# Kernel tuning notes

Measured on AMD Instinct MI355X. Metric: run time of the kernel, lower is better.

## Reference

```python
import jax, jax.numpy as jnp
import numpy as np

N_NODES = 50000
IN_CH = 512
OUT_CH = 512
N_EDGES = 800000


def setup_inputs() -> dict:
    key = jax.random.key(0)
    ks = jax.random.split(key, 6)
    x = jax.random.normal(ks[0], (N_NODES, IN_CH), dtype=jnp.float32)
    edge_index = jax.random.randint(ks[1], (2, N_EDGES), 0, N_NODES, dtype=jnp.int64)
    edge_index_2 = jax.random.randint(ks[2], (2, N_EDGES), 0, N_NODES, dtype=jnp.int64)
    W1 = jax.random.normal(ks[3], (IN_CH, OUT_CH), dtype=jnp.float32) * (1.0 / np.sqrt(IN_CH))
    b1 = jnp.zeros((OUT_CH,), dtype=jnp.float32)
    W2 = jax.random.normal(ks[4], (IN_CH, OUT_CH), dtype=jnp.float32) * (1.0 / np.sqrt(IN_CH))
    b2 = jnp.zeros((OUT_CH,), dtype=jnp.float32)
    return {"x": x, "edge_index": edge_index, "edge_index_2": edge_index_2,
            "W1": W1, "b1": b1, "W2": W2, "b2": b2}


def _sgconv(x, edge_index, W, b, K=2):
    # PyG SGConv: K rounds of D^-1/2 (A+I) D^-1/2 propagation, then Linear.
    N = x.shape[0]
    loops = jnp.arange(N, dtype=edge_index.dtype)
    row = jnp.concatenate([edge_index[0], loops])  # source nodes
    col = jnp.concatenate([edge_index[1], loops])  # destination nodes
    deg = jax.ops.segment_sum(jnp.ones_like(col, dtype=x.dtype), col, num_segments=N)
    deg_inv_sqrt = jnp.where(deg > 0, jnp.where(deg > 0, deg, 1.0) ** -0.5, 0.0)
    norm = deg_inv_sqrt[row] * deg_inv_sqrt[col]  # [E+N]
    h = x
    for _ in range(K):
        h = jax.ops.segment_sum(h[row] * norm[:, None], col, num_segments=N)
    return h @ W + b


def reference(x, edge_index, edge_index_2, W1, b1, W2, b2):
    x1 = _sgconv(x, edge_index, W1, b1)
    x2 = _sgconv(x, edge_index_2, W2, b2)
    logits = jax.nn.softmax(x1, axis=1)
    logits_2 = jax.nn.softmax(x2, axis=1)
    predictions = jnp.argmax(logits, axis=1)
    return (logits, logits_2, predictions)
```

## Files before the change

### kernel.cpp

```cpp
#include <hip/hip_runtime.h>
#include <hip/hip_bf16.h>
#include <cstdint>
#include <cstddef>

#define N_NODES 50000
#define N_EDGES 800000
#define CH 512

typedef __attribute__((ext_vector_type(8))) short bf16x8;
typedef __attribute__((ext_vector_type(4))) float f32x4;

__device__ inline unsigned short f2b(float f) {
    __hip_bfloat16 h = __float2bfloat16(f);
    return *(unsigned short*)&h;
}
__device__ inline float blo(unsigned int u) {
    union { unsigned int i; float f; } v; v.i = u << 16; return v.f;
}
__device__ inline float bhi(unsigned int u) {
    union { unsigned int i; float f; } v; v.i = u & 0xffff0000u; return v.f;
}
__device__ inline unsigned int pack2(unsigned short a, unsigned short b) {
    return (unsigned)a | ((unsigned)b << 16);
}


__global__ __launch_bounds__(256) void count_col(const int* __restrict__ col, int* __restrict__ cnt) {
    int e = blockIdx.x * 256 + threadIdx.x;
    if (e < N_EDGES) atomicAdd(&cnt[col[e]], 1);
}

__global__ __launch_bounds__(1024) void scan_offsets(const int* __restrict__ cnt, int* __restrict__ offs,
                                                     float* __restrict__ dinv) {
    __shared__ int wsum[16];
    __shared__ int s_carry;
    int tid = threadIdx.x;
    int lane = tid & 63, wid = tid >> 6;
    if (tid == 0) s_carry = 0;
    __syncthreads();
    const int n = N_NODES;
    for (int c0 = 0; c0 < n; c0 += 1024) {
        int i = c0 + tid;
        int v = (i < n) ? cnt[i] : 0;
        if (i < n) dinv[i] = rsqrtf((float)(v + 1));
        int incl = v;
        #pragma unroll
        for (int d = 1; d < 64; d <<= 1) {
            int t = __shfl_up(incl, d, 64);
            if (lane >= d) incl += t;
        }
        if (lane == 63) wsum[wid] = incl;
        __syncthreads();
        int wbase = 0;
        for (int w = 0; w < wid; ++w) wbase += wsum[w];
        int excl = s_carry + wbase + incl - v;
        if (i < n) offs[i] = excl;
        int ctot = wbase + incl;
        __syncthreads();
        if (tid == 1023) s_carry += ctot;
        __syncthreads();
    }
    if (tid == 0) offs[n] = s_carry;
}

__global__ __launch_bounds__(256) void fill_csr(const int* __restrict__ edges,
                                                const int* __restrict__ offs,
                                                int* __restrict__ cursor,
                                                const float* __restrict__ dinv,
                                                int* __restrict__ srcs,
                                                float* __restrict__ enorm) {
    int e = blockIdx.x * 256 + threadIdx.x;
    if (e >= N_EDGES) return;
    int r = edges[e];
    int c = edges[N_EDGES + e];
    int p = offs[c] + atomicAdd(&cursor[c], 1);
    srcs[p] = r;
    enorm[p] = dinv[r] * dinv[c];
}


__global__ __launch_bounds__(256) void convert_x_bf16(const float* __restrict__ x, unsigned short* __restrict__ xb) {
    int i8 = blockIdx.x * 256 + threadIdx.x;
    const float4* x4 = (const float4*)x;
    float4 a = x4[2 * i8], b = x4[2 * i8 + 1];
    unsigned int o[4];
    o[0] = pack2(f2b(a.x), f2b(a.y));
    o[1] = pack2(f2b(a.z), f2b(a.w));
    o[2] = pack2(f2b(b.x), f2b(b.y));
    o[3] = pack2(f2b(b.z), f2b(b.w));
    ((uint4*)xb)[i8] = make_uint4(o[0], o[1], o[2], o[3]);
}

__global__ __launch_bounds__(256) void convert_w_t(const float* __restrict__ W, unsigned short* __restrict__ Wt) {
    int id = blockIdx.x * 256 + threadIdx.x;
    int k = id >> 9, n = id & 511;
    Wt[(size_t)n * 512 + k] = f2b(W[(size_t)k * 512 + n]);
}

__global__ __launch_bounds__(256) void convert_w_t_split(const float* __restrict__ W,
                                                         unsigned short* __restrict__ Wth,
                                                         unsigned short* __restrict__ Wtl) {
    int id = blockIdx.x * 256 + threadIdx.x;
    int k = id >> 9, n = id & 511;
    float f = W[(size_t)k * 512 + n];
    unsigned short hb = f2b(f);
    union { unsigned int u; float ff; } t; t.u = (unsigned)hb << 16;
    float lo = f - t.ff;
    Wth[(size_t)n * 512 + k] = hb;
    Wtl[(size_t)n * 512 + k] = f2b(lo);
}


__global__ __launch_bounds__(128) void propagate(const float* __restrict__ h, float* __restrict__ out,
                                                 const int* __restrict__ offs,
                                                 const int* __restrict__ srcs,
                                                 const float* __restrict__ enorm,
                                                 const float* __restrict__ dinv) {
    int node = blockIdx.x;
    int t = threadIdx.x;
    const float4* h4 = (const float4*)h;
    float di = dinv[node];
    float w0 = di * di;
    float4 v = h4[(size_t)node * 128 + t];
    float4 acc = make_float4(v.x * w0, v.y * w0, v.z * w0, v.w * w0);
    int e0 = offs[node], e1 = offs[node + 1];
    int e = e0;
    int eu = e0 + ((e1 - e0) & ~7);
    for (; e < eu; e += 8) {
        int s[8]; float w[8];
        #pragma unroll
        for (int q = 0; q < 8; ++q) { s[q] = srcs[e + q]; w[q] = enorm[e + q]; }
        float4 u[8];
        #pragma unroll
        for (int q = 0; q < 8; ++q) u[q] = h4[(size_t)s[q] * 128 + t];
        #pragma unroll
        for (int q = 0; q < 8; ++q) {
            acc.x += u[q].x * w[q]; acc.y += u[q].y * w[q];
            acc.z += u[q].z * w[q]; acc.w += u[q].w * w[q];
        }
    }
    for (; e < e1; ++e) {
        int s = srcs[e];
        float w = enorm[e];
        float4 u = h4[(size_t)s * 128 + t];
        acc.x += u.x * w; acc.y += u.y * w; acc.z += u.z * w; acc.w += u.w * w;
    }
    ((float4*)out)[(size_t)node * 128 + t] = acc;
}


__global__ __launch_bounds__(128) void propagate_bf16(const unsigned short* __restrict__ hb,
                                                      unsigned short* __restrict__ outb,
                                                      const int* __restrict__ offs,
                                                      const int* __restrict__ srcs,
                                                      const float* __restrict__ enorm,
                                                      const float* __restrict__ dinv) {
    int node = blockIdx.x * 2 + (threadIdx.x >> 6);
    int lane = threadIdx.x & 63;
    const uint4* h16 = (const uint4*)hb;
    float di = dinv[node];
    float w0 = di * di;
    float acc[8];
    uint4 sv = h16[(size_t)node * 64 + lane];
    acc[0] = blo(sv.x) * w0; acc[1] = bhi(sv.x) * w0;
    acc[2] = blo(sv.y) * w0; acc[3] = bhi(sv.y) * w0;
    acc[4] = blo(sv.z) * w0; acc[5] = bhi(sv.z) * w0;
    acc[6] = blo(sv.w) * w0; acc[7] = bhi(sv.w) * w0;
    int e0 = offs[node], e1 = offs[node + 1];
    int e = e0;
    int eu = e0 + ((e1 - e0) & ~7);
    for (; e < eu; e += 8) {
        int s[8]; float w[8];
        #pragma unroll
        for (int q = 0; q < 8; ++q) { s[q] = srcs[e + q]; w[q] = enorm[e + q]; }
        uint4 u[8];
        #pragma unroll
        for (int q = 0; q < 8; ++q) u[q] = h16[(size_t)s[q] * 64 + lane];
        #pragma unroll
        for (int q = 0; q < 8; ++q) {
            acc[0] += blo(u[q].x) * w[q]; acc[1] += bhi(u[q].x) * w[q];
            acc[2] += blo(u[q].y) * w[q]; acc[3] += bhi(u[q].y) * w[q];
            acc[4] += blo(u[q].z) * w[q]; acc[5] += bhi(u[q].z) * w[q];
            acc[6] += blo(u[q].w) * w[q]; acc[7] += bhi(u[q].w) * w[q];
        }
    }
    for (; e < e1; ++e) {
        int s = srcs[e];
        float w = enorm[e];
        uint4 u = h16[(size_t)s * 64 + lane];
        acc[0] += blo(u.x) * w; acc[1] += bhi(u.x) * w;
        acc[2] += blo(u.y) * w; acc[3] += bhi(u.y) * w;
        acc[4] += blo(u.z) * w; acc[5] += bhi(u.z) * w;
        acc[6] += blo(u.w) * w; acc[7] += bhi(u.w) * w;
    }
    unsigned int o0 = pack2(f2b(acc[0]), f2b(acc[1]));
    unsigned int o1 = pack2(f2b(acc[2]), f2b(acc[3]));
    unsigned int o2 = pack2(f2b(acc[4]), f2b(acc[5]));
    unsigned int o3 = pack2(f2b(acc[6]), f2b(acc[7]));
    ((uint4*)outb)[(size_t)node * 64 + lane] = make_uint4(o0, o1, o2, o3);
}


#define BM2 128
#define BN2 256
#define BK2 32
#define LDP 40

__global__ __launch_bounds__(512) void gemm_bf16(const unsigned short* __restrict__ Ab,
                                                 const unsigned short* __restrict__ Wt,
                                                 const float* __restrict__ bias,
                                                 float* __restrict__ C) {
    __shared__ short Alds[BM2 * LDP];
    __shared__ short Blds[BN2 * LDP];
    int tid = threadIdx.x;
    int lane = tid & 63;
    int wid = tid >> 6;
    int wm = wid & 1;
    int wn = wid >> 1;
    int bm = blockIdx.x * BM2;
    int bn = blockIdx.y * BN2;

    f32x4 acc[4][4] = {};

    int arow = tid >> 2, ak8 = (tid & 3) * 8;
    int brow = tid >> 1, bk16 = (tid & 1) * 16;
    int ga = bm + arow;
    bool aval = ga < N_NODES;

    for (int k0 = 0; k0 < CH; k0 += BK2) {
        {
            uint4 v = make_uint4(0u, 0u, 0u, 0u);
            if (aval) v = *(const uint4*)&Ab[(size_t)ga * CH + k0 + ak8];
            *(uint4*)&Alds[arow * LDP + ak8] = v;
        }
        {
            const unsigned short* s = &Wt[(size_t)(bn + brow) * CH + k0 + bk16];
            *(uint4*)&Blds[brow * LDP + bk16] = *(const uint4*)s;
            *(uint4*)&Blds[brow * LDP + bk16 + 8] = *(const uint4*)(s + 8);
        }
        __syncthreads();

        bf16x8 af[4], bf[4];
        #pragma unroll
        for (int mt = 0; mt < 4; ++mt)
            af[mt] = *(const bf16x8*)&Alds[(wm * 64 + mt * 16 + (lane & 15)) * LDP + (lane >> 4) * 8];
        #pragma unroll
        for (int nt = 0; nt < 4; ++nt)
            bf[nt] = *(const bf16x8*)&Blds[(wn * 64 + nt * 16 + (lane & 15)) * LDP + (lane >> 4) * 8];
        #pragma unroll
        for (int mt = 0; mt < 4; ++mt)
            #pragma unroll
            for (int nt = 0; nt < 4; ++nt)
                acc[mt][nt] = __builtin_amdgcn_mfma_f32_16x16x32_bf16(af[mt], bf[nt], acc[mt][nt], 0, 0, 0);
        __syncthreads();
    }

    #pragma unroll
    for (int mt = 0; mt < 4; ++mt) {
        #pragma unroll
        for (int nt = 0; nt < 4; ++nt) {
            int col = bn + wn * 64 + nt * 16 + (lane & 15);
            float bv = bias[col];
            #pragma unroll
            for (int r = 0; r < 4; ++r) {
                int row = bm + wm * 64 + mt * 16 + (lane >> 4) * 4 + r;
                if (row < N_NODES) C[(size_t)row * CH + col] = acc[mt][nt][r] + bv;
            }
        }
    }
}


#define BM3 128
#define BN3 256
#define BK3 32
#define LDP3 40

__global__ __launch_bounds__(512) void gemm_bf16x3(const float* __restrict__ A,
                                                   const unsigned short* __restrict__ Wth,
                                                   const unsigned short* __restrict__ Wtl,
                                                   const float* __restrict__ bias,
                                                   float* __restrict__ C) {
    __shared__ short Ah[BM3 * LDP3];
    __shared__ short Al[BM3 * LDP3];
    __shared__ short Bh[BN3 * LDP3];
    __shared__ short Bl[BN3 * LDP3];
    int tid = threadIdx.x;
    int lane = tid & 63;
    int wid = tid >> 6;
    int wm = wid & 1;
    int wn = wid >> 1;
    int bm = blockIdx.x * BM3;
    int bn = blockIdx.y * BN3;

    f32x4 acc[4][4] = {};

    int arow = tid >> 2, ak8 = (tid & 3) * 8;
    int brow = tid >> 1, bk16 = (tid & 1) * 16;
    int ga = bm + arow;
    bool aval = ga < N_NODES;

    for (int k0 = 0; k0 < CH; k0 += BK3) {
        {
            const float* src = &A[(size_t)ga * CH + k0 + ak8];
            float4 f0 = aval ? *(const float4*)(src)     : make_float4(0.f, 0.f, 0.f, 0.f);
            float4 f1 = aval ? *(const float4*)(src + 4) : make_float4(0.f, 0.f, 0.f, 0.f);
            float fs[8] = {f0.x, f0.y, f0.z, f0.w, f1.x, f1.y, f1.z, f1.w};
            unsigned short h[8], l[8];
            #pragma unroll
            for (int j = 0; j < 8; ++j) {
                unsigned short hb = f2b(fs[j]);
                union { unsigned int u; float ff; } t; t.u = (unsigned)hb << 16;
                float lo = fs[j] - t.ff;
                h[j] = hb;
                l[j] = f2b(lo);
            }
            *(uint4*)&Ah[arow * LDP3 + ak8] =
                make_uint4(pack2(h[0], h[1]), pack2(h[2], h[3]), pack2(h[4], h[5]), pack2(h[6], h[7]));
            *(uint4*)&Al[arow * LDP3 + ak8] =
                make_uint4(pack2(l[0], l[1]), pack2(l[2], l[3]), pack2(l[4], l[5]), pack2(l[6], l[7]));
        }
        {
            const unsigned short* sh = &Wth[(size_t)(bn + brow) * CH + k0 + bk16];
            const unsigned short* sl = &Wtl[(size_t)(bn + brow) * CH + k0 + bk16];
            *(uint4*)&Bh[brow * LDP3 + bk16]     = *(const uint4*)sh;
            *(uint4*)&Bh[brow * LDP3 + bk16 + 8] = *(const uint4*)(sh + 8);
            *(uint4*)&Bl[brow * LDP3 + bk16]     = *(const uint4*)sl;
            *(uint4*)&Bl[brow * LDP3 + bk16 + 8] = *(const uint4*)(sl + 8);
        }
        __syncthreads();

        bf16x8 afh[4], afl[4], bfh[4], bfl[4];
        #pragma unroll
        for (int mt = 0; mt < 4; ++mt) {
            int off = (wm * 64 + mt * 16 + (lane & 15)) * LDP3 + (lane >> 4) * 8;
            afh[mt] = *(const bf16x8*)&Ah[off];
            afl[mt] = *(const bf16x8*)&Al[off];
        }
        #pragma unroll
        for (int nt = 0; nt < 4; ++nt) {
            int off = (wn * 64 + nt * 16 + (lane & 15)) * LDP3 + (lane >> 4) * 8;
            bfh[nt] = *(const bf16x8*)&Bh[off];
            bfl[nt] = *(const bf16x8*)&Bl[off];
        }
        #pragma unroll
        for (int mt = 0; mt < 4; ++mt)
            #pragma unroll
            for (int nt = 0; nt < 4; ++nt) {
                acc[mt][nt] = __builtin_amdgcn_mfma_f32_16x16x32_bf16(afh[mt], bfh[nt], acc[mt][nt], 0, 0, 0);
                acc[mt][nt] = __builtin_amdgcn_mfma_f32_16x16x32_bf16(afl[mt], bfh[nt], acc[mt][nt], 0, 0, 0);
                acc[mt][nt] = __builtin_amdgcn_mfma_f32_16x16x32_bf16(afh[mt], bfl[nt], acc[mt][nt], 0, 0, 0);
            }
        __syncthreads();
    }

    #pragma unroll
    for (int mt = 0; mt < 4; ++mt) {
        #pragma unroll
        for (int nt = 0; nt < 4; ++nt) {
            int col = bn + wn * 64 + nt * 16 + (lane & 15);
            float bv = bias[col];
            #pragma unroll
            for (int r = 0; r < 4; ++r) {
                int row = bm + wm * 64 + mt * 16 + (lane >> 4) * 4 + r;
                if (row < N_NODES) C[(size_t)row * CH + col] = acc[mt][nt][r] + bv;
            }
        }
    }
}


#define GAP_THR 2.0e-4f
#define SUSP_CAP 49999

__global__ __launch_bounds__(256) void softmax_rows(const float* __restrict__ X, float* __restrict__ P,
                                                    float* __restrict__ preds,
                                                    int* __restrict__ susp_cnt,
                                                    int* __restrict__ susp_rows) {
    int row = blockIdx.x * 4 + (threadIdx.x >> 6);
    int lane = threadIdx.x & 63;
    if (row >= N_NODES) return;
    const float4* x4 = (const float4*)(X + (size_t)row * CH);
    float4 v0 = x4[lane];
    float4 v1 = x4[lane + 64];
    float vals[8] = {v0.x, v0.y, v0.z, v0.w, v1.x, v1.y, v1.z, v1.w};
    float m = vals[0];
    float m2 = -INFINITY;
    int mi = lane * 4;
    #pragma unroll
    for (int j = 1; j < 8; ++j) {
        int c = (j < 4) ? (lane * 4 + j) : (256 + lane * 4 + (j - 4));
        if (vals[j] > m) { m2 = m; m = vals[j]; mi = c; }
        else if (vals[j] > m2) { m2 = vals[j]; }
    }
    #pragma unroll
    for (int d = 32; d > 0; d >>= 1) {
        float om = __shfl_xor(m, d, 64);
        int oi = __shfl_xor(mi, d, 64);
        float om2 = __shfl_xor(m2, d, 64);
        if (om > m || (om == m && oi < mi)) {
            m2 = fmaxf(m, om2);
            m = om; mi = oi;
        } else {
            m2 = fmaxf(m2, om);
        }
    }
    float s = 0.f;
    float ex[8];
    #pragma unroll
    for (int j = 0; j < 8; ++j) { ex[j] = __expf(vals[j] - m); s += ex[j]; }
    #pragma unroll
    for (int d = 32; d > 0; d >>= 1) s += __shfl_xor(s, d, 64);
    float inv = 1.0f / s;
    float4 o0 = make_float4(ex[0] * inv, ex[1] * inv, ex[2] * inv, ex[3] * inv);
    float4 o1 = make_float4(ex[4] * inv, ex[5] * inv, ex[6] * inv, ex[7] * inv);
    float4* p4 = (float4*)(P + (size_t)row * CH);
    p4[lane] = o0;
    p4[lane + 64] = o1;
    if (preds != nullptr && lane == 0) {
        preds[row] = (float)mi;
        if (m - m2 < GAP_THR) {
            int p = atomicAdd(susp_cnt, 1);
            if (p < SUSP_CAP) susp_rows[p] = row;
        }
    }
}


__global__ __launch_bounds__(256) void fix_preds(const float* __restrict__ A, const float* __restrict__ W,
                                                 const float* __restrict__ bias,
                                                 const int* __restrict__ susp_cnt,
                                                 const int* __restrict__ susp_rows,
                                                 float* __restrict__ preds) {
    __shared__ float rowbuf[8][512];
    __shared__ float rbest[8][4];
    __shared__ int ridx[8][4];
    int cnt = *susp_cnt;
    if (cnt > SUSP_CAP) cnt = SUSP_CAP;
    int tid = threadIdx.x, lane = tid & 63, wid = tid >> 6;
    for (int base = blockIdx.x * 8; base < cnt; base += gridDim.x * 8) {
        int nr = min(8, cnt - base);
        __syncthreads();
        for (int r = 0; r < nr; ++r) {
            int row = susp_rows[base + r];
            if (tid < 128) ((float4*)rowbuf[r])[tid] = ((const float4*)&A[(size_t)row * 512])[tid];
        }
        __syncthreads();
        float best[8]; int bidx[8];
        #pragma unroll
        for (int r = 0; r < 8; ++r) { best[r] = -INFINITY; bidx[r] = 0; }
        for (int cc = 0; cc < 2; ++cc) {
            int c = cc * 256 + tid;
            float bv = bias[c];
            float s[8];
            #pragma unroll
            for (int r = 0; r < 8; ++r) s[r] = bv;
            #pragma unroll 8
            for (int k = 0; k < 512; ++k) {
                float w = W[(size_t)k * 512 + c];
                #pragma unroll
                for (int r = 0; r < 8; ++r) s[r] += rowbuf[r][k] * w;
            }
            #pragma unroll
            for (int r = 0; r < 8; ++r)
                if (s[r] > best[r]) { best[r] = s[r]; bidx[r] = c; }
        }
        #pragma unroll
        for (int r = 0; r < 8; ++r) {
            float b = best[r]; int i = bidx[r];
            #pragma unroll
            for (int d = 32; d > 0; d >>= 1) {
                float ob = __shfl_xor(b, d, 64);
                int oi = __shfl_xor(i, d, 64);
                if (ob > b || (ob == b && oi < i)) { b = ob; i = oi; }
            }
            if (lane == 0) { rbest[r][wid] = b; ridx[r][wid] = i; }
        }
        __syncthreads();
        if (tid < nr) {
            int r = tid;
            float b = rbest[r][0]; int i = ridx[r][0];
            #pragma unroll
            for (int w = 1; w < 4; ++w) {
                if (rbest[r][w] > b || (rbest[r][w] == b && ridx[r][w] < i)) { b = rbest[r][w]; i = ridx[r][w]; }
            }
            preds[susp_rows[base + r]] = (float)i;
        }
    }
}


extern "C" void kernel_launch(void* const* d_in, const int* in_sizes, int n_in,
                              void* d_out, int out_size, void* d_ws, size_t ws_size,
                              hipStream_t stream) {
    const float* x  = (const float*)d_in[0];
    const int*   e1 = (const int*)d_in[1];
    const int*   e2 = (const int*)d_in[2];
    const float* W1 = (const float*)d_in[3];
    const float* b1 = (const float*)d_in[4];
    const float* W2 = (const float*)d_in[5];
    const float* b2 = (const float*)d_in[6];

    float* out     = (float*)d_out;
    float* logits1 = out;
    float* logits2 = out + (size_t)N_NODES * CH;
    float* preds   = out + 2 * (size_t)N_NODES * CH;

    const size_t NEED = 109600016;
    if (ws_size < NEED) return;

    char* ws = (char*)d_ws;
    float* A      = (float*)(ws);
    int*   cnt    = (int*)(ws + 102400000);
    int*   offs   = (int*)(ws + 102600000);
    int*   cursor = (int*)(ws + 102800016);
    float* dinv   = (float*)(ws + 103000016);
    int*   srcs   = (int*)(ws + 103200016);
    float* enorm  = (float*)(ws + 106400016);

    unsigned short* xb  = (unsigned short*)logits1;
    unsigned short* Wtb = (unsigned short*)((char*)logits1 + 51200000);
    unsigned short* h1b = (unsigned short*)A;
    unsigned short* h2b = (unsigned short*)((char*)A + 51200000);

    unsigned short* Wt1h = (unsigned short*)srcs;
    unsigned short* Wt1l = (unsigned short*)enorm;
    int* susp_cnt  = (int*)cursor;
    int* susp_rows = (int*)cursor + 1;

    {
        hipMemsetAsync(cnt, 0, N_NODES * sizeof(int), stream);
        hipMemsetAsync(cursor, 0, N_NODES * sizeof(int), stream);
        count_col<<<(N_EDGES + 255) / 256, 256, 0, stream>>>(e2 + N_EDGES, cnt);
        scan_offsets<<<1, 1024, 0, stream>>>(cnt, offs, dinv);
        fill_csr<<<(N_EDGES + 255) / 256, 256, 0, stream>>>(e2, offs, cursor, dinv, srcs, enorm);

        convert_x_bf16<<<(N_NODES * CH / 8 + 255) / 256, 256, 0, stream>>>(x, xb);
        convert_w_t<<<(512 * 512) / 256, 256, 0, stream>>>(W2, Wtb);

        propagate_bf16<<<N_NODES / 2, 128, 0, stream>>>(xb, h1b, offs, srcs, enorm, dinv);
        propagate_bf16<<<N_NODES / 2, 128, 0, stream>>>(h1b, h2b, offs, srcs, enorm, dinv);

        dim3 g((N_NODES + BM2 - 1) / BM2, CH / BN2);
        gemm_bf16<<<g, 512, 0, stream>>>(h2b, Wtb, b2, logits2);
        softmax_rows<<<N_NODES / 4, 256, 0, stream>>>(logits2, logits2, nullptr, nullptr, nullptr);
    }

    {
        hipMemsetAsync(cnt, 0, N_NODES * sizeof(int), stream);
        hipMemsetAsync(cursor, 0, N_NODES * sizeof(int), stream);
        count_col<<<(N_EDGES + 255) / 256, 256, 0, stream>>>(e1 + N_EDGES, cnt);
        scan_offsets<<<1, 1024, 0, stream>>>(cnt, offs, dinv);
        fill_csr<<<(N_EDGES + 255) / 256, 256, 0, stream>>>(e1, offs, cursor, dinv, srcs, enorm);

        propagate<<<N_NODES, 128, 0, stream>>>(x, logits1, offs, srcs, enorm, dinv);
        propagate<<<N_NODES, 128, 0, stream>>>(logits1, A, offs, srcs, enorm, dinv);

        convert_w_t_split<<<(512 * 512) / 256, 256, 0, stream>>>(W1, Wt1h, Wt1l);
        hipMemsetAsync(susp_cnt, 0, sizeof(int), stream);

        dim3 g((N_NODES + BM3 - 1) / BM3, CH / BN3);
        gemm_bf16x3<<<g, 512, 0, stream>>>(A, Wt1h, Wt1l, b1, logits1);
        softmax_rows<<<N_NODES / 4, 256, 0, stream>>>(logits1, logits1, preds, susp_cnt, susp_rows);
        fix_preds<<<400, 256, 0, stream>>>(A, W1, b1, susp_cnt, susp_rows, preds);
    }
}
```

Measured before the change: 1.676 ms.

## Build both graphs' CSR together with a multi-block parallel scan

Replaces the single-block, 1024-thread serial-chunk prefix scan with a three-stage multi-block scan. The stages are a per-block scan, a scan of the block sums, and an add-back fused with the dinv computation and the cursor reset. The count and fill kernels for both edge sets are merged into single launches, with graph 2's CSR arrays placed in the not-yet-written logits2 output buffer. This removes a serialized single-CU scan and several launches and memsets. It relies on logits2 staying untouched until graph 2's propagation has finished.

```diff
diff --git a/kernel.cpp b/kernel.cpp
--- a/kernel.cpp
+++ b/kernel.cpp
@@ -6,6 +6,7 @@
 #define N_NODES 50000
 #define N_EDGES 800000
 #define CH 512
+#define SCAN_NB 49
 
 typedef __attribute__((ext_vector_type(8))) short bf16x8;
 typedef __attribute__((ext_vector_type(4))) float f32x4;
@@ -25,57 +26,108 @@
 }
 
 
-__global__ __launch_bounds__(256) void count_col(const int* __restrict__ col, int* __restrict__ cnt) {
-    int e = blockIdx.x * 256 + threadIdx.x;
-    if (e < N_EDGES) atomicAdd(&cnt[col[e]], 1);
-}
-
-__global__ __launch_bounds__(1024) void scan_offsets(const int* __restrict__ cnt, int* __restrict__ offs,
-                                                     float* __restrict__ dinv) {
-    __shared__ int wsum[16];
-    __shared__ int s_carry;
-    int tid = threadIdx.x;
+__global__ __launch_bounds__(256) void count_both(const int* __restrict__ e1, const int* __restrict__ e2,
+                                                  int* __restrict__ cnt1, int* __restrict__ cnt2) {
+    int t = blockIdx.x * 256 + threadIdx.x;
+    if (t < N_EDGES) {
+        atomicAdd(&cnt1[e1[N_EDGES + t]], 1);
+    } else if (t < 2 * N_EDGES) {
+        int e = t - N_EDGES;
+        atomicAdd(&cnt2[e2[N_EDGES + e]], 1);
+    }
+}
+
+__global__ __launch_bounds__(256) void scan_s1(const int* __restrict__ c1, const int* __restrict__ c2,
+                                               int* __restrict__ o1, int* __restrict__ o2,
+                                               int* __restrict__ bsum) {
+    const int* cnt = blockIdx.y ? c2 : c1;
+    int* offs = blockIdx.y ? o2 : o1;
+    int* bs = bsum + blockIdx.y * 64;
+    int b = blockIdx.x, tid = threadIdx.x;
     int lane = tid & 63, wid = tid >> 6;
-    if (tid == 0) s_carry = 0;
+    int i0 = b * 1024 + tid * 4;
+    int v[4];
+    #pragma unroll
+    for (int j = 0; j < 4; ++j) { int i = i0 + j; v[j] = (i < N_NODES) ? cnt[i] : 0; }
+    int tsum = v[0] + v[1] + v[2] + v[3];
+    int incl = tsum;
+    #pragma unroll
+    for (int d = 1; d < 64; d <<= 1) {
+        int t = __shfl_up(incl, d, 64);
+        if (lane >= d) incl += t;
+    }
+    __shared__ int wsum[4];
+    if (lane == 63) wsum[wid] = incl;
     __syncthreads();
-    const int n = N_NODES;
-    for (int c0 = 0; c0 < n; c0 += 1024) {
-        int i = c0 + tid;
-        int v = (i < n) ? cnt[i] : 0;
-        if (i < n) dinv[i] = rsqrtf((float)(v + 1));
-        int incl = v;
-        #pragma unroll
-        for (int d = 1; d < 64; d <<= 1) {
-            int t = __shfl_up(incl, d, 64);
-            if (lane >= d) incl += t;
-        }
-        if (lane == 63) wsum[wid] = incl;
-        __syncthreads();
-        int wbase = 0;
-        for (int w = 0; w < wid; ++w) wbase += wsum[w];
-        int excl = s_carry + wbase + incl - v;
-        if (i < n) offs[i] = excl;
-        int ctot = wbase + incl;
-        __syncthreads();
-        if (tid == 1023) s_carry += ctot;
-        __syncthreads();
-    }
-    if (tid == 0) offs[n] = s_carry;
-}
-
-__global__ __launch_bounds__(256) void fill_csr(const int* __restrict__ edges,
-                                                const int* __restrict__ offs,
-                                                int* __restrict__ cursor,
-                                                const float* __restrict__ dinv,
-                                                int* __restrict__ srcs,
-                                                float* __restrict__ enorm) {
-    int e = blockIdx.x * 256 + threadIdx.x;
-    if (e >= N_EDGES) return;
-    int r = edges[e];
-    int c = edges[N_EDGES + e];
-    int p = offs[c] + atomicAdd(&cursor[c], 1);
-    srcs[p] = r;
-    enorm[p] = dinv[r] * dinv[c];
+    int wbase = 0;
+    for (int w = 0; w < wid; ++w) wbase += wsum[w];
+    int run = wbase + incl - tsum;
+    #pragma unroll
+    for (int j = 0; j < 4; ++j) { int i = i0 + j; if (i < N_NODES) offs[i] = run; run += v[j]; }
+    if (tid == 255) bs[b] = wbase + incl;
+}
+
+__global__ __launch_bounds__(64) void scan_s2(int* __restrict__ bsum,
+                                              int* __restrict__ o1, int* __restrict__ o2) {
+    int* bs = bsum + blockIdx.y * 64;
+    int* offs = blockIdx.y ? o2 : o1;
+    int t = threadIdx.x;
+    int v = (t < SCAN_NB) ? bs[t] : 0;
+    int incl = v;
+    #pragma unroll
+    for (int d = 1; d < 64; d <<= 1) {
+        int u = __shfl_up(incl, d, 64);
+        if (t >= d) incl += u;
+    }
+    if (t < SCAN_NB) bs[t] = incl - v;
+    if (t == 63) offs[N_NODES] = incl;
+}
+
+__global__ __launch_bounds__(256) void scan_s3(const int* __restrict__ c1, const int* __restrict__ c2,
+                                               int* __restrict__ o1, int* __restrict__ o2,
+                                               float* __restrict__ d1, float* __restrict__ d2,
+                                               int* __restrict__ cur1, int* __restrict__ cur2,
+                                               const int* __restrict__ bsum) {
+    const int* cnt = blockIdx.y ? c2 : c1;
+    int* offs = blockIdx.y ? o2 : o1;
+    float* dinv = blockIdx.y ? d2 : d1;
+    int* cursor = blockIdx.y ? cur2 : cur1;
+    int add = bsum[blockIdx.y * 64 + blockIdx.x];
+    int i0 = blockIdx.x * 1024 + threadIdx.x * 4;
+    #pragma unroll
+    for (int j = 0; j < 4; ++j) {
+        int i = i0 + j;
+        if (i < N_NODES) {
+            offs[i] += add;
+            dinv[i] = rsqrtf((float)(cnt[i] + 1));
+            cursor[i] = 0;
+        }
+    }
+}
+
+__global__ __launch_bounds__(256) void fill_both(const int* __restrict__ e1,
+                                                 const int* __restrict__ offs1, int* __restrict__ cur1,
+                                                 const float* __restrict__ dinv1,
+                                                 int* __restrict__ srcs1, float* __restrict__ enorm1,
+                                                 const int* __restrict__ e2,
+                                                 const int* __restrict__ offs2, int* __restrict__ cur2,
+                                                 const float* __restrict__ dinv2,
+                                                 int* __restrict__ srcs2, float* __restrict__ enorm2) {
+    int t = blockIdx.x * 256 + threadIdx.x;
+    if (t < N_EDGES) {
+        int r = e1[t];
+        int c = e1[N_EDGES + t];
+        int p = offs1[c] + atomicAdd(&cur1[c], 1);
+        srcs1[p] = r;
+        enorm1[p] = dinv1[r] * dinv1[c];
+    } else if (t < 2 * N_EDGES) {
+        int e = t - N_EDGES;
+        int r = e2[e];
+        int c = e2[N_EDGES + e];
+        int p = offs2[c] + atomicAdd(&cur2[c], 1);
+        srcs2[p] = r;
+        enorm2[p] = dinv2[r] * dinv2[c];
+    }
 }
 
 
@@ -510,36 +562,52 @@
     if (ws_size < NEED) return;
 
     char* ws = (char*)d_ws;
-    float* A      = (float*)(ws);
-    int*   cnt    = (int*)(ws + 102400000);
-    int*   offs   = (int*)(ws + 102600000);
-    int*   cursor = (int*)(ws + 102800016);
-    float* dinv   = (float*)(ws + 103000016);
-    int*   srcs   = (int*)(ws + 103200016);
-    float* enorm  = (float*)(ws + 106400016);
+    float* A       = (float*)(ws);
+    int*   cnt1    = (int*)(ws + 102400000);
+    int*   offs1   = (int*)(ws + 102600000);
+    int*   cursor1 = (int*)(ws + 102800016);
+    float* dinv1   = (float*)(ws + 103000016);
+    int*   srcs1   = (int*)(ws + 103200016);
+    float* enorm1  = (float*)(ws + 106400016);
+
+    char* L2 = (char*)logits2;
+    int*   cnt2    = (int*)(L2);
+    int*   offs2   = (int*)(L2 + 200000);
+    int*   cursor2 = (int*)(L2 + 400016);
+    float* dinv2   = (float*)(L2 + 600016);
+    int*   srcs2   = (int*)(L2 + 800016);
+    float* enorm2  = (float*)(L2 + 4000016);
+    int*   bsum    = (int*)(L2 + 7200016);
 
     unsigned short* xb  = (unsigned short*)logits1;
     unsigned short* Wtb = (unsigned short*)((char*)logits1 + 51200000);
     unsigned short* h1b = (unsigned short*)A;
     unsigned short* h2b = (unsigned short*)((char*)A + 51200000);
 
-    unsigned short* Wt1h = (unsigned short*)srcs;
-    unsigned short* Wt1l = (unsigned short*)enorm;
-    int* susp_cnt  = (int*)cursor;
-    int* susp_rows = (int*)cursor + 1;
+    unsigned short* Wt1h = (unsigned short*)srcs1;
+    unsigned short* Wt1l = (unsigned short*)enorm1;
+    int* susp_cnt  = (int*)cursor1;
+    int* susp_rows = (int*)cursor1 + 1;
 
     {
-        hipMemsetAsync(cnt, 0, N_NODES * sizeof(int), stream);
-        hipMemsetAsync(cursor, 0, N_NODES * sizeof(int), stream);
-        count_col<<<(N_EDGES + 255) / 256, 256, 0, stream>>>(e2 + N_EDGES, cnt);
-        scan_offsets<<<1, 1024, 0, stream>>>(cnt, offs, dinv);
-        fill_csr<<<(N_EDGES + 255) / 256, 256, 0, stream>>>(e2, offs, cursor, dinv, srcs, enorm);
-
+        hipMemsetAsync(cnt1, 0, N_NODES * sizeof(int), stream);
+        hipMemsetAsync(cnt2, 0, N_NODES * sizeof(int), stream);
+        count_both<<<(2 * N_EDGES + 255) / 256, 256, 0, stream>>>(e1, e2, cnt1, cnt2);
+        scan_s1<<<dim3(SCAN_NB, 2), 256, 0, stream>>>(cnt1, cnt2, offs1, offs2, bsum);
+        scan_s2<<<dim3(1, 2), 64, 0, stream>>>(bsum, offs1, offs2);
+        scan_s3<<<dim3(SCAN_NB, 2), 256, 0, stream>>>(cnt1, cnt2, offs1, offs2,
+                                                      dinv1, dinv2, cursor1, cursor2, bsum);
+        fill_both<<<(2 * N_EDGES + 255) / 256, 256, 0, stream>>>(
+            e1, offs1, cursor1, dinv1, srcs1, enorm1,
+            e2, offs2, cursor2, dinv2, srcs2, enorm2);
+    }
+
+    {
         convert_x_bf16<<<(N_NODES * CH / 8 + 255) / 256, 256, 0, stream>>>(x, xb);
         convert_w_t<<<(512 * 512) / 256, 256, 0, stream>>>(W2, Wtb);
 
-        propagate_bf16<<<N_NODES / 2, 128, 0, stream>>>(xb, h1b, offs, srcs, enorm, dinv);
-        propagate_bf16<<<N_NODES / 2, 128, 0, stream>>>(h1b, h2b, offs, srcs, enorm, dinv);
+        propagate_bf16<<<N_NODES / 2, 128, 0, stream>>>(xb, h1b, offs2, srcs2, enorm2, dinv2);
+        propagate_bf16<<<N_NODES / 2, 128, 0, stream>>>(h1b, h2b, offs2, srcs2, enorm2, dinv2);
 
         dim3 g((N_NODES + BM2 - 1) / BM2, CH / BN2);
         gemm_bf16<<<g, 512, 0, stream>>>(h2b, Wtb, b2, logits2);
@@ -547,14 +615,8 @@
     }
 
     {
-        hipMemsetAsync(cnt, 0, N_NODES * sizeof(int), stream);
-        hipMemsetAsync(cursor, 0, N_NODES * sizeof(int), stream);
-        count_col<<<(N_EDGES + 255) / 256, 256, 0, stream>>>(e1 + N_EDGES, cnt);
-        scan_offsets<<<1, 1024, 0, stream>>>(cnt, offs, dinv);
-        fill_csr<<<(N_EDGES + 255) / 256, 256, 0, stream>>>(e1, offs, cursor, dinv, srcs, enorm);
-
-        propagate<<<N_NODES, 128, 0, stream>>>(x, logits1, offs, srcs, enorm, dinv);
-        propagate<<<N_NODES, 128, 0, stream>>>(logits1, A, offs, srcs, enorm, dinv);
+        propagate<<<N_NODES, 128, 0, stream>>>(x, logits1, offs1, srcs1, enorm1, dinv1);
+        propagate<<<N_NODES, 128, 0, stream>>>(logits1, A, offs1, srcs1, enorm1, dinv1);
 
         convert_w_t_split<<<(512 * 512) / 256, 256, 0, stream>>>(W1, Wt1h, Wt1l);
         hipMemsetAsync(susp_cnt, 0, sizeof(int), stream);
```

Measured after the change: 1.561 ms. 6.9% less time.
